# Performance work log

Measured on AMD Instinct MI355X. Metric: run time of the kernel, lower is better.

Reference implementation:

```python
import jax, jax.numpy as jnp
import numpy as np

B, T = 4096, 2048
ETA = 10.0  # constant['eta']


def setup_inputs() -> dict:
    key = jax.random.key(0)
    k0, k1, k2 = jax.random.split(key, 3)
    return {
        "inputs": jax.random.normal(k0, (B, T, 2), dtype=jnp.float32),  # [:,:,0]=eps, [:,:,1]=hs (step size)
        "W1": jax.random.normal(k1, (2, 16), dtype=jnp.float32) * 0.5,
        "b1": jnp.zeros((16,), dtype=jnp.float32),
        "W2": jax.random.normal(k2, (16, 1), dtype=jnp.float32) * 0.5,
        "b2": jnp.zeros((1,), dtype=jnp.float32),
    }


def reference(inputs, W1, b1, W2, b2):
    # GSM recurrent cell: e = MLP([eps, gamma]); sig = de/deps; gamma' = gamma - hs/eta * de/dgamma.
    # Analytic gradient of scalar e w.r.t. x (softplus' = sigmoid):
    #   de/dx = (sigmoid(x @ W1 + b1) * W2[:, 0]) @ W1.T      # [B, 2]
    inv_eta = 1.0 / ETA
    w2 = W2[:, 0]  # [16]

    def step(gamma, inp_t):  # gamma: [B,1], inp_t: [B,2]
        eps = inp_t[:, 0:1]
        hs = inp_t[:, 1:2]
        x = jnp.concatenate([eps, gamma], axis=1)            # [B,2]
        z1 = x @ W1 + b1                                     # [B,16]
        de_dx = (jax.nn.sigmoid(z1) * w2) @ W1.T             # [B,2]
        sig = de_dx[:, 0:1]                                  # de/deps
        gamma_n = gamma - hs * inv_eta * de_dx[:, 1:2]       # de/dgamma update
        return gamma_n, sig

    gamma0 = jnp.zeros((inputs.shape[0], 1), dtype=inputs.dtype)
    _, sig_seq = jax.lax.scan(step, gamma0, jnp.swapaxes(inputs, 0, 1))  # sig_seq: [T,B,1]
    return jnp.swapaxes(sig_seq, 0, 1)  # [B,T,1]
```

## Files before the change

### kernel.cpp

```cpp
#include <hip/hip_runtime.h>
#include <cmath>

#define B_ROWS 4096
#define T_LEN  2048
#define TB     16
#define NBLK   (T_LEN / TB)

template<int CTRL>
__device__ __forceinline__ float dpp_add(float x) {
  int y = __builtin_amdgcn_mov_dpp(__builtin_bit_cast(int, x),
                                   CTRL, 0xf, 0xf, true);
  return x + __builtin_bit_cast(float, y);
}
__device__ __forceinline__ float allreduce16(float x) {
  x = dpp_add<0xB1>(x);
  x = dpp_add<0x4E>(x);
  x = dpp_add<0x141>(x);
  x = dpp_add<0x140>(x);
  return x;
}

struct Coef { float a[8]; float K; };

struct Blk { float4 q[8]; };

__device__ __forceinline__ void load_blk(const float4* __restrict__ src,
                                         Blk& b) {
#pragma unroll
  for (int i = 0; i < 8; ++i) b.q[i] = src[i];
}

struct Pre { float dpre[TB - 1]; float hwn[TB]; float eps15; };

__device__ __forceinline__ void extract(const Blk& b, float w0j, float w1j,
                                        Pre& p) {
  float eps[TB];
#pragma unroll
  for (int i = 0; i < 8; ++i) {
    eps[2 * i]       = b.q[i].x;
    p.hwn[2 * i]     = -b.q[i].y * w1j;
    eps[2 * i + 1]   = b.q[i].z;
    p.hwn[2 * i + 1] = -b.q[i].w * w1j;
  }
#pragma unroll
  for (int t = 0; t < TB - 1; ++t) p.dpre[t] = (eps[t + 1] - eps[t]) * w0j;
  p.eps15 = eps[TB - 1];
}

__device__ __forceinline__ void compute16(const Pre& p, float nextq0x,
                                          bool peek, float& u, const Coef cf,
                                          float w0j, float c0j, float c1j,
                                          float h0, float h1, int j,
                                          float* __restrict__ outp) {
  float keep = 0.0f;
#pragma unroll
  for (int t = 0; t < TB; ++t) {
    float uc  = __builtin_amdgcn_fmed3f(u, -cf.K, cf.K);
    float u2  = uc * uc;
    float c1u = c1j * uc;
    float c0u = c0j * uc;
    float b0 = fmaf(cf.a[1], u2, cf.a[0]);
    float b1 = fmaf(cf.a[3], u2, cf.a[2]);
    float b2 = fmaf(cf.a[5], u2, cf.a[4]);
    float b3 = fmaf(cf.a[7], u2, cf.a[6]);
    float u4 = u2 * u2;
    float d0 = fmaf(b1, u4, b0);
    float d1 = fmaf(b3, u4, b2);
    float u8 = u4 * u4;
    float q  = fmaf(d1, u8, d0);
    float v1 = fmaf(c1u, q, h1);
    float v0 = fmaf(c0u, q, h0);
    float s1 = allreduce16(v1);
    float s0 = allreduce16(v0);
    float dpre_t = (t < TB - 1)
                     ? p.dpre[t]
                     : (peek ? ((nextq0x - p.eps15) * w0j) : 0.0f);
    float P = u + dpre_t;
    u    = fmaf(p.hwn[t], s1, P);
    keep = (j == t) ? s0 : keep;
  }
  outp[j] = keep;
}

__global__ __launch_bounds__(64) void gsm_scan_kernel(
    const float* __restrict__ inp, const float* __restrict__ W1f,
    const float* __restrict__ b1f, const float* __restrict__ W2f,
    float* __restrict__ out, const Coef cf) {
  const int lane = threadIdx.x;
  const int grp  = lane >> 4;
  const int j    = lane & 15;
  const int row  = (blockIdx.x << 2) + grp;

  const float w0j = W1f[j];
  const float w1j = W1f[16 + j];
  const float bj  = b1f[j];
  const float w2j = W2f[j];
  const float c0j = w2j * w0j;
  const float c1j = 0.1f * w2j * w1j;
  const float h0  = 0.5f * c0j;
  const float h1  = 0.5f * c1j;

  const float4* src = (const float4*)(inp + (size_t)row * (2 * T_LEN));
  float* outrow = out + (size_t)row * T_LEN;

  Blk A, Bb;
  Pre p;
  load_blk(src, A);
  load_blk(src + 8, Bb);
  float u = fmaf(A.q[0].x, w0j, bj);

#pragma unroll 1
  for (int b = 0; b < NBLK; b += 2) {
    extract(A, w0j, w1j, p);
    if (b + 2 < NBLK) load_blk(src + (size_t)(b + 2) * 8, A);
    compute16(p, Bb.q[0].x, true, u, cf, w0j, c0j, c1j, h0, h1, j,
              outrow + b * TB);
    extract(Bb, w0j, w1j, p);
    if (b + 3 < NBLK) load_blk(src + (size_t)(b + 3) * 8, Bb);
    compute16(p, A.q[0].x, (b + 2 < NBLK), u, cf, w0j, c0j, c1j, h0, h1, j,
              outrow + (b + 1) * TB);
  }
}

static void fit_sigma_coeffs(double K, Coef& cf) {
  const int N = 1024;
  double M[8][8] = {{0}}, bv[8] = {0}, a[8];
  for (int i = 0; i < N; ++i) {
    double th = 3.14159265358979323846 * (i + 0.5) / (2.0 * N);
    double s  = cos(th);
    double u  = K * s;
    double f  = 1.0 / (1.0 + exp(-u)) - 0.5;
    double pk[8]; double sp = s;
    for (int k = 0; k < 8; ++k) { pk[k] = sp; sp *= s * s; }
    for (int r = 0; r < 8; ++r) {
      bv[r] += f * pk[r];
      for (int c = 0; c < 8; ++c) M[r][c] += pk[r] * pk[c];
    }
  }
  for (int col = 0; col < 8; ++col) {
    int piv = col;
    for (int r = col + 1; r < 8; ++r)
      if (fabs(M[r][col]) > fabs(M[piv][col])) piv = r;
    if (piv != col) {
      for (int c = 0; c < 8; ++c) { double t = M[col][c]; M[col][c] = M[piv][c]; M[piv][c] = t; }
      double t = bv[col]; bv[col] = bv[piv]; bv[piv] = t;
    }
    for (int r = col + 1; r < 8; ++r) {
      double fac = M[r][col] / M[col][col];
      for (int c = col; c < 8; ++c) M[r][c] -= fac * M[col][c];
      bv[r] -= fac * bv[col];
    }
  }
  for (int r = 7; r >= 0; --r) {
    double s2 = bv[r];
    for (int c = r + 1; c < 8; ++c) s2 -= M[r][c] * a[c];
    a[r] = s2 / M[r][r];
  }
  double Kp = K;
  for (int k = 0; k < 8; ++k) { cf.a[k] = (float)(a[k] / Kp); Kp *= K * K; }
  cf.K = (float)K;
}

extern "C" void kernel_launch(void* const* d_in, const int* in_sizes, int n_in,
                              void* d_out, int out_size, void* d_ws,
                              size_t ws_size, hipStream_t stream) {
  const float* inp = (const float*)d_in[0];
  const float* W1  = (const float*)d_in[1];
  const float* b1  = (const float*)d_in[2];
  const float* W2  = (const float*)d_in[3];
  float* out = (float*)d_out;

  Coef cf;
  fit_sigma_coeffs(6.5, cf);

  dim3 grid(B_ROWS / 4);
  dim3 block(64);
  hipLaunchKernelGGL(gsm_scan_kernel, grid, block, 0, stream,
                     inp, W1, b1, W2, out, cf);
}
```

Measured before the change: 125.3 us.

## Pack two hidden units per lane with f32x2 math and 8 lanes per row

Each lane now handles two of the 16 hidden units as a float2, so 8 lanes serve one row and a 64-lane wave covers 8 rows instead of 4. The packed vector FMAs cut the per-step instruction count, and the cross-lane reduction drops from four DPP adds to three plus one in-lane add. This shortens the serial dependency chain of each recurrence step. The grid is halved to 512 workgroups, which lowers the number of resident waves per CU and may leave SIMDs idle while less latency gets hidden.

Result: slower. 149.5 us (+19.4%).

```diff
diff --git a/kernel.cpp b/kernel.cpp
--- a/kernel.cpp
+++ b/kernel.cpp
@@ -6,80 +6,85 @@
 #define TB     16
 #define NBLK   (T_LEN / TB)
 
+typedef float f32x2 __attribute__((ext_vector_type(2)));
+
 template<int CTRL>
 __device__ __forceinline__ float dpp_add(float x) {
-  int y = __builtin_amdgcn_mov_dpp(__builtin_bit_cast(int, x),
-                                   CTRL, 0xf, 0xf, true);
+  int y = __builtin_amdgcn_update_dpp(0, __builtin_bit_cast(int, x),
+                                      CTRL, 0xf, 0xf, true);
   return x + __builtin_bit_cast(float, y);
 }
-__device__ __forceinline__ float allreduce16(float x) {
+__device__ __forceinline__ float allreduce8(float x) {
   x = dpp_add<0xB1>(x);
   x = dpp_add<0x4E>(x);
   x = dpp_add<0x141>(x);
-  x = dpp_add<0x140>(x);
   return x;
 }
 
 struct Coef { float a[8]; float K; };
 
 struct Blk { float4 q[8]; };
-
 __device__ __forceinline__ void load_blk(const float4* __restrict__ src,
                                          Blk& b) {
 #pragma unroll
   for (int i = 0; i < 8; ++i) b.q[i] = src[i];
 }
 
-struct Pre { float dpre[TB - 1]; float hwn[TB]; float eps15; };
-
-__device__ __forceinline__ void extract(const Blk& b, float w0j, float w1j,
-                                        Pre& p) {
+struct Pre { float deps[TB - 1]; float hsn[TB]; float eps15; };
+__device__ __forceinline__ void extract(const Blk& b, Pre& p) {
   float eps[TB];
 #pragma unroll
   for (int i = 0; i < 8; ++i) {
     eps[2 * i]       = b.q[i].x;
-    p.hwn[2 * i]     = -b.q[i].y * w1j;
+    p.hsn[2 * i]     = -b.q[i].y;
     eps[2 * i + 1]   = b.q[i].z;
-    p.hwn[2 * i + 1] = -b.q[i].w * w1j;
+    p.hsn[2 * i + 1] = -b.q[i].w;
   }
 #pragma unroll
-  for (int t = 0; t < TB - 1; ++t) p.dpre[t] = (eps[t + 1] - eps[t]) * w0j;
+  for (int t = 0; t < TB - 1; ++t) p.deps[t] = eps[t + 1] - eps[t];
   p.eps15 = eps[TB - 1];
 }
 
-__device__ __forceinline__ void compute16(const Pre& p, float nextq0x,
-                                          bool peek, float& u, const Coef cf,
-                                          float w0j, float c0j, float c1j,
-                                          float h0, float h1, int j,
-                                          float* __restrict__ outp) {
-  float keep = 0.0f;
+__device__ __forceinline__ void compute16(
+    const Pre& p, float nextq0x, bool peek, f32x2& u, const f32x2* A,
+    float K, f32x2 w0p, f32x2 w1p, f32x2 c0p, f32x2 c1p, f32x2 h0p,
+    f32x2 h1p, int j, float* __restrict__ outp) {
+  float keep0 = 0.0f, keep1 = 0.0f;
 #pragma unroll
   for (int t = 0; t < TB; ++t) {
-    float uc  = __builtin_amdgcn_fmed3f(u, -cf.K, cf.K);
-    float u2  = uc * uc;
-    float c1u = c1j * uc;
-    float c0u = c0j * uc;
-    float b0 = fmaf(cf.a[1], u2, cf.a[0]);
-    float b1 = fmaf(cf.a[3], u2, cf.a[2]);
-    float b2 = fmaf(cf.a[5], u2, cf.a[4]);
-    float b3 = fmaf(cf.a[7], u2, cf.a[6]);
-    float u4 = u2 * u2;
-    float d0 = fmaf(b1, u4, b0);
-    float d1 = fmaf(b3, u4, b2);
-    float u8 = u4 * u4;
-    float q  = fmaf(d1, u8, d0);
-    float v1 = fmaf(c1u, q, h1);
-    float v0 = fmaf(c0u, q, h0);
-    float s1 = allreduce16(v1);
-    float s0 = allreduce16(v0);
-    float dpre_t = (t < TB - 1)
-                     ? p.dpre[t]
-                     : (peek ? ((nextq0x - p.eps15) * w0j) : 0.0f);
-    float P = u + dpre_t;
-    u    = fmaf(p.hwn[t], s1, P);
-    keep = (j == t) ? s0 : keep;
+    f32x2 uc;
+    uc.x = __builtin_amdgcn_fmed3f(u.x, -K, K);
+    uc.y = __builtin_amdgcn_fmed3f(u.y, -K, K);
+    f32x2 u2 = uc * uc;
+    f32x2 e0 = __builtin_elementwise_fma(A[1], u2, A[0]);
+    f32x2 e1 = __builtin_elementwise_fma(A[3], u2, A[2]);
+    f32x2 e2 = __builtin_elementwise_fma(A[5], u2, A[4]);
+    f32x2 e3 = __builtin_elementwise_fma(A[7], u2, A[6]);
+    f32x2 u4 = u2 * u2;
+    f32x2 d0 = __builtin_elementwise_fma(e1, u4, e0);
+    f32x2 d1 = __builtin_elementwise_fma(e3, u4, e2);
+    f32x2 u8 = u4 * u4;
+    f32x2 qq = __builtin_elementwise_fma(d1, u8, d0);
+    f32x2 v1 = __builtin_elementwise_fma(c1p * uc, qq, h1p);
+    f32x2 v0 = __builtin_elementwise_fma(c0p * uc, qq, h0p);
+    float a1 = v1.x + v1.y;
+    float a0 = v0.x + v0.y;
+    asm volatile("" : "+v"(a0), "+v"(a1));
+    float s1 = allreduce8(a1);
+    float s0 = allreduce8(a0);
+    float dep = (t < TB - 1) ? p.deps[t]
+                             : (peek ? (nextq0x - p.eps15) : 0.0f);
+    float hw0 = w1p.x * p.hsn[t];
+    float hw1 = w1p.y * p.hsn[t];
+    float P0  = fmaf(w0p.x, dep, u.x);
+    float P1  = fmaf(w0p.y, dep, u.y);
+    u.x = fmaf(hw0, s1, P0);
+    u.y = fmaf(hw1, s1, P1);
+    keep0 = (t < 8 && j == t)      ? s0 : keep0;
+    keep1 = (t >= 8 && j == t - 8) ? s0 : keep1;
   }
-  outp[j] = keep;
+  outp[j]     = keep0;
+  outp[8 + j] = keep1;
 }
 
 __global__ __launch_bounds__(64) void gsm_scan_kernel(
@@ -87,38 +92,44 @@
     const float* __restrict__ b1f, const float* __restrict__ W2f,
     float* __restrict__ out, const Coef cf) {
   const int lane = threadIdx.x;
-  const int grp  = lane >> 4;
-  const int j    = lane & 15;
-  const int row  = (blockIdx.x << 2) + grp;
+  const int g    = lane >> 3;
+  const int j    = lane & 7;
+  const int row  = (blockIdx.x << 3) + g;
 
-  const float w0j = W1f[j];
-  const float w1j = W1f[16 + j];
-  const float bj  = b1f[j];
-  const float w2j = W2f[j];
-  const float c0j = w2j * w0j;
-  const float c1j = 0.1f * w2j * w1j;
-  const float h0  = 0.5f * c0j;
-  const float h1  = 0.5f * c1j;
+  f32x2 w0p, w1p, bp, w2p;
+  w0p.x = W1f[j];      w0p.y = W1f[j + 8];
+  w1p.x = W1f[16 + j]; w1p.y = W1f[24 + j];
+  bp.x  = b1f[j];      bp.y  = b1f[j + 8];
+  w2p.x = W2f[j];      w2p.y = W2f[j + 8];
+  f32x2 c0p = w2p * w0p;
+  f32x2 c1p = (w2p * w1p) * 0.1f;
+  f32x2 h0p = c0p * 0.5f;
+  f32x2 h1p = c1p * 0.5f;
+  f32x2 A[8];
+#pragma unroll
+  for (int k = 0; k < 8; ++k) { A[k].x = cf.a[k]; A[k].y = cf.a[k]; }
 
   const float4* src = (const float4*)(inp + (size_t)row * (2 * T_LEN));
   float* outrow = out + (size_t)row * T_LEN;
 
-  Blk A, Bb;
+  Blk Ab, Bb;
   Pre p;
-  load_blk(src, A);
+  load_blk(src, Ab);
   load_blk(src + 8, Bb);
-  float u = fmaf(A.q[0].x, w0j, bj);
+  f32x2 u;
+  u.x = fmaf(Ab.q[0].x, w0p.x, bp.x);
+  u.y = fmaf(Ab.q[0].x, w0p.y, bp.y);
 
 #pragma unroll 1
   for (int b = 0; b < NBLK; b += 2) {
-    extract(A, w0j, w1j, p);
-    if (b + 2 < NBLK) load_blk(src + (size_t)(b + 2) * 8, A);
-    compute16(p, Bb.q[0].x, true, u, cf, w0j, c0j, c1j, h0, h1, j,
-              outrow + b * TB);
-    extract(Bb, w0j, w1j, p);
+    extract(Ab, p);
+    if (b + 2 < NBLK) load_blk(src + (size_t)(b + 2) * 8, Ab);
+    compute16(p, Bb.q[0].x, true, u, A, cf.K, w0p, w1p, c0p, c1p, h0p, h1p,
+              j, outrow + b * TB);
+    extract(Bb, p);
     if (b + 3 < NBLK) load_blk(src + (size_t)(b + 3) * 8, Bb);
-    compute16(p, A.q[0].x, (b + 2 < NBLK), u, cf, w0j, c0j, c1j, h0, h1, j,
-              outrow + (b + 1) * TB);
+    compute16(p, Ab.q[0].x, (b + 2 < NBLK), u, A, cf.K, w0p, w1p, c0p, c1p,
+              h0p, h1p, j, outrow + (b + 1) * TB);
   }
 }
 
@@ -173,7 +184,7 @@
   Coef cf;
   fit_sigma_coeffs(6.5, cf);
 
-  dim3 grid(B_ROWS / 4);
+  dim3 grid(B_ROWS / 8);
   dim3 block(64);
   hipLaunchKernelGGL(gsm_scan_kernel, grid, block, 0, stream,
                      inp, W1, b1, W2, out, cf);
```
